# Kernel tuning notes

Hardware: AMD Instinct MI355X
Metric: run time of the kernel (lower is better)

Reference implementation:

```python
import jax, jax.numpy as jnp
import numpy as np

N, E, F, H, G, C, L = 50000, 800000, 128, 256, 128, 10, 3


def _gcn(x, src, dst, norm, W, b, n):
    # PyG GCNConv: h = x W; out_i = sum_{j->i} norm_ji h_j (+ self loops already in src/dst); + bias
    h = x @ W
    msg = h[src] * norm[:, None]              # [E+N, H]
    return jax.ops.segment_sum(msg, dst, num_segments=n) + b


def setup_inputs() -> dict:
    key = jax.random.key(0)
    ks = jax.random.split(key, 8)
    x = jax.random.normal(ks[0], (N, F), dtype=jnp.float32)
    edge_index = jax.random.randint(ks[1], (2, E), 0, N, dtype=jnp.int32)
    batch = jnp.sort(jax.random.randint(ks[2], (N,), 0, G, dtype=jnp.int32))
    graph_hidden = jax.random.normal(ks[3], (G, H), dtype=jnp.float32)
    W0 = jax.random.normal(ks[4], (F, H), dtype=jnp.float32) / np.sqrt(F)
    b0 = jnp.zeros((H,), jnp.float32)
    Ws = jax.random.normal(ks[5], (L, H, H), dtype=jnp.float32) / np.sqrt(H)
    bs = jnp.zeros((L, H), jnp.float32)
    Wlin = jax.random.normal(ks[6], (H, C), dtype=jnp.float32) / np.sqrt(H)
    blin = jnp.zeros((C,), jnp.float32)
    return {"x": x, "edge_index": edge_index, "batch": batch, "graph_hidden": graph_hidden,
            "W0": W0, "b0": b0, "Ws": Ws, "bs": bs, "Wlin": Wlin, "blin": blin}


def reference(x, edge_index, batch, graph_hidden, W0, b0, Ws, bs, Wlin, blin):
    n = x.shape[0]
    loops = jnp.arange(n, dtype=edge_index.dtype)
    src = jnp.concatenate([edge_index[0], loops])   # self loops appended
    dst = jnp.concatenate([edge_index[1], loops])
    deg = jax.ops.segment_sum(jnp.ones_like(src, dtype=x.dtype), dst, num_segments=n)
    inv_sqrt = jnp.where(deg > 0, jax.lax.rsqrt(deg), 0.0)
    norm = inv_sqrt[src] * inv_sqrt[dst]            # [E+N]

    h = _gcn(x, src, dst, norm, W0, b0, n)          # to_hidden (no activation, matches source)
    res = jax.lax.stop_gradient(graph_hidden[batch])  # no_grad residual, vectorized
    for i in range(Ws.shape[0]):
        h = h + res
        h = jax.nn.relu(_gcn(h, src, dst, norm, Ws[i], bs[i], n))
        # dropout is identity in eval mode

    counts = jax.ops.segment_sum(jnp.ones((n,), x.dtype), batch, num_segments=G)
    gm = jax.ops.segment_sum(h, batch, num_segments=G) / jnp.maximum(counts, 1.0)[:, None]
    gm = gm + graph_hidden
    y = gm @ Wlin + blin
    return (y, gm)
```

## Files before the change

kernel.cpp:

```cpp
#include <hip/hip_runtime.h>


typedef float f32x4 __attribute__((ext_vector_type(4)));
typedef float f32x2 __attribute__((ext_vector_type(2)));

__device__ inline float bf2f(unsigned short u) {
  union { unsigned int i; float f; } v;
  v.i = (unsigned int)u << 16;
  return v.f;
}
__device__ inline unsigned short f2bf(float f) {
  union { unsigned int i; float f; } v;
  v.f = f;
  unsigned int i = v.i;
  return (unsigned short)((i + 0x7fffu + ((i >> 16) & 1u)) >> 16);
}
__device__ inline unsigned pack4_fp8(float a, float b, float c, float d) {
  int r = 0;
  r = __builtin_amdgcn_cvt_pk_fp8_f32(a, b, r, false);
  r = __builtin_amdgcn_cvt_pk_fp8_f32(c, d, r, true);
  return (unsigned)r;
}
__device__ inline unsigned char f2fp8(float v) {
  return (unsigned char)((unsigned)__builtin_amdgcn_cvt_pk_fp8_f32(v, v, 0, false) & 0xffu);
}
__device__ inline void acc16_fp8(float* acc, uint4 r, unsigned msk) {
  unsigned w[4] = {r.x, r.y, r.z, r.w};
#pragma unroll
  for (int d = 0; d < 4; ++d) {
    int v = (int)(w[d] & msk);
    f32x2 lo = __builtin_amdgcn_cvt_pk_f32_fp8(v, false);
    f32x2 hi = __builtin_amdgcn_cvt_pk_f32_fp8(v, true);
    acc[4 * d + 0] += lo[0];
    acc[4 * d + 1] += lo[1];
    acc[4 * d + 2] += hi[0];
    acc[4 * d + 3] += hi[1];
  }
}
__device__ inline int lbound(const int* a, int n, int key) {
  int lo = 0, hi = n;
  while (lo < hi) {
    int mid = (lo + hi) >> 1;
    if (a[mid] < key) lo = mid + 1; else hi = mid;
  }
  return lo;
}


__global__ void count_pos_kernel(const int* __restrict__ dst, int* __restrict__ deg,
                                 unsigned short* __restrict__ pos, int E) {
  int e = blockIdx.x * blockDim.x + threadIdx.x;
  if (e < E) pos[e] = (unsigned short)atomicAdd(&deg[dst[e]], 1);
}

__global__ void scan_partial_kernel(const int* __restrict__ deg, float* __restrict__ inv_s,
                                    int* __restrict__ bsum, int N) {
  __shared__ int s[256];
  int i = blockIdx.x * 256 + threadIdx.x;
  int d = (i < N) ? deg[i] : 0;
  if (i < N) inv_s[i] = rsqrtf((float)(d + 1));
  s[threadIdx.x] = d;
  __syncthreads();
  for (int off = 128; off > 0; off >>= 1) {
    if (threadIdx.x < off) s[threadIdx.x] += s[threadIdx.x + off];
    __syncthreads();
  }
  if (threadIdx.x == 0) bsum[blockIdx.x] = s[0];
}

__global__ void scan_block_kernel(const int* __restrict__ bsum, int* __restrict__ boff,
                                  int* __restrict__ row_off, int NB, int N) {
  __shared__ int s[256];
  int v = (threadIdx.x < NB) ? bsum[threadIdx.x] : 0;
  s[threadIdx.x] = v;
  __syncthreads();
  for (int off = 1; off < 256; off <<= 1) {
    int t = (threadIdx.x >= off) ? s[threadIdx.x - off] : 0;
    __syncthreads();
    s[threadIdx.x] += t;
    __syncthreads();
  }
  boff[threadIdx.x] = s[threadIdx.x] - v;
  if (threadIdx.x == 255) row_off[N] = s[255];
}

__global__ void scan_final_kernel(const int* __restrict__ deg, const int* __restrict__ boff,
                                  int* __restrict__ row_off, int N) {
  __shared__ int s[256];
  int i = blockIdx.x * 256 + threadIdx.x;
  int v = (i < N) ? deg[i] : 0;
  s[threadIdx.x] = v;
  __syncthreads();
  for (int off = 1; off < 256; off <<= 1) {
    int t = (threadIdx.x >= off) ? s[threadIdx.x - off] : 0;
    __syncthreads();
    s[threadIdx.x] += t;
    __syncthreads();
  }
  if (i < N) row_off[i] = boff[blockIdx.x] + s[threadIdx.x] - v;
}

__global__ void fill_prep_kernel(const int* __restrict__ src, const int* __restrict__ dst,
                                 const unsigned short* __restrict__ pos,
                                 const int* __restrict__ row_off, int* __restrict__ col, int E,
                                 int FB, const float* __restrict__ x,
                                 const float* __restrict__ inv_s, unsigned* __restrict__ u,
                                 int total_dw, const float* __restrict__ W0,
                                 const float* __restrict__ Ws, unsigned char* __restrict__ Wt0,
                                 unsigned char* __restrict__ WtS) {
  const int FH = 128 * 256, HH = 256 * 256;
  int b = blockIdx.x;
  if (b < FB) {
    int t = b * 256 + threadIdx.x;
    int e = t * 4;
    if (e + 3 < E) {
      int4 s4 = *(const int4*)&src[e];
      int4 d4 = *(const int4*)&dst[e];
      ushort4 p4 = *(const ushort4*)&pos[e];
      col[row_off[d4.x] + p4.x] = s4.x;
      col[row_off[d4.y] + p4.y] = s4.y;
      col[row_off[d4.z] + p4.z] = s4.z;
      col[row_off[d4.w] + p4.w] = s4.w;
    } else {
      for (; e < E; ++e) col[row_off[dst[e]] + pos[e]] = src[e];
    }
  } else {
    int idx = (b - FB) * 256 + threadIdx.x;
    if (idx < total_dw) {
      int i = idx >> 5;
      float s = inv_s[i];
      float4 v = *(const float4*)&x[(size_t)idx * 4];
      u[idx] = pack4_fp8(s * v.x, s * v.y, s * v.z, s * v.w);
    } else {
      int w = idx - total_dw;
      if (w < FH) {
        int k = w >> 8, n = w & 255;
        Wt0[n * 128 + k] = f2fp8(W0[w]);
      } else {
        int t2 = w - FH;
        if (t2 < 3 * HH) {
          int l = t2 >> 16;
          int rem = t2 & 65535;
          int k = rem >> 8, n = rem & 255;
          WtS[l * HH + n * 256 + k] = f2fp8(Ws[t2]);
        }
      }
    }
  }
}

template <int CH>
__global__ __launch_bounds__(256) void aggregate_fp8_kernel(
    const unsigned char* __restrict__ u, const int* __restrict__ row_off,
    const int* __restrict__ col, const float* __restrict__ inv_s,
    unsigned char* __restrict__ out, int N) {
  constexpr int LPR = CH / 16;
  constexpr int EPW = 64 / LPR;
  int wave = threadIdx.x >> 6;
  int lane = threadIdx.x & 63;
  int i = blockIdx.x * 4 + wave;
  if (i >= N) return;
  int sub = lane / LPR;
  int c = lane % LPR;
  int e0 = row_off[i], e1 = row_off[i + 1];
  int last = e1 - 1;
  float acc[16] = {};
  for (int e = e0 + sub; e < e1; e += 4 * EPW) {
    unsigned off[4];
    unsigned msk[4];
#pragma unroll
    for (int q = 0; q < 4; ++q) {
      int ee = e + q * EPW;
      bool v = ee < e1;
      int j = col[v ? ee : last];
      off[q] = (unsigned)j * CH + c * 16;
      msk[q] = v ? 0xffffffffu : 0u;
    }
    uint4 r[4];
#pragma unroll
    for (int q = 0; q < 4; ++q) r[q] = *(const uint4*)(u + off[q]);
#pragma unroll
    for (int q = 0; q < 4; ++q) acc16_fp8(acc, r[q], msk[q]);
  }
#pragma unroll
  for (int o = 32; o >= LPR; o >>= 1)
#pragma unroll
    for (int k = 0; k < 16; ++k) acc[k] += __shfl_down(acc[k], o);
  if (lane < LPR) {
    uint4 self = *(const uint4*)(u + (size_t)i * CH + c * 16);
    acc16_fp8(acc, self, 0xffffffffu);
    float s = inv_s[i];
    uint4 o;
    o.x = pack4_fp8(s * acc[0], s * acc[1], s * acc[2], s * acc[3]);
    o.y = pack4_fp8(s * acc[4], s * acc[5], s * acc[6], s * acc[7]);
    o.z = pack4_fp8(s * acc[8], s * acc[9], s * acc[10], s * acc[11]);
    o.w = pack4_fp8(s * acc[12], s * acc[13], s * acc[14], s * acc[15]);
    *(uint4*)(out + (size_t)i * CH + c * 16) = o;
  }
}

__global__ __launch_bounds__(256) void aggregate_fp8_ns_kernel(
    const unsigned char* __restrict__ u, const int* __restrict__ row_off,
    const int* __restrict__ col, const float* __restrict__ inv_s,
    unsigned char* __restrict__ out, int N) {
  constexpr int CH = 256;
  int slice = blockIdx.x & 1;
  int nb = blockIdx.x >> 1;
  int lane = threadIdx.x & 63;
  int wave = threadIdx.x >> 6;
  int grp = lane >> 3;
  int c = lane & 7;
  int i = nb * 32 + wave * 8 + grp;
  if (i >= N) return;
  int e0 = row_off[i], e1 = row_off[i + 1];
  int last = e1 - 1;
  unsigned sofs = (unsigned)slice * 128 + c * 16;
  float acc[16] = {};
  for (int e = e0; e < e1; e += 4) {
    unsigned off[4];
    unsigned msk[4];
#pragma unroll
    for (int q = 0; q < 4; ++q) {
      int ee = e + q;
      bool v = ee < e1;
      int j = col[v ? ee : last];
      off[q] = (unsigned)j * CH + sofs;
      msk[q] = v ? 0xffffffffu : 0u;
    }
    uint4 r[4];
#pragma unroll
    for (int q = 0; q < 4; ++q) r[q] = *(const uint4*)(u + off[q]);
#pragma unroll
    for (int q = 0; q < 4; ++q) acc16_fp8(acc, r[q], msk[q]);
  }
  uint4 self = *(const uint4*)(u + (size_t)i * CH + sofs);
  acc16_fp8(acc, self, 0xffffffffu);
  float s = inv_s[i];
  uint4 o;
  o.x = pack4_fp8(s * acc[0], s * acc[1], s * acc[2], s * acc[3]);
  o.y = pack4_fp8(s * acc[4], s * acc[5], s * acc[6], s * acc[7]);
  o.z = pack4_fp8(s * acc[8], s * acc[9], s * acc[10], s * acc[11]);
  o.w = pack4_fp8(s * acc[12], s * acc[13], s * acc[14], s * acc[15]);
  *(uint4*)(out + (size_t)i * CH + sofs) = o;
}

template <int K, bool RELU, int OUTMODE>
__global__ __launch_bounds__(512) void gemm_kernel(
    const unsigned char* __restrict__ A,
    const unsigned char* __restrict__ Bt,
    const float* __restrict__ bias,
    const float* __restrict__ inv_s, const int* __restrict__ batch,
    const float* __restrict__ gh,
    void* __restrict__ outp,
    int M) {
  constexpr int BK = 64;
  constexpr int LDT = 80;
  __shared__ unsigned char As[128 * LDT];
  __shared__ unsigned char Bs[256 * LDT];
  int tid = threadIdx.x;
  int wave = tid >> 6, lane = tid & 63;
  int quad = lane >> 4, l15 = lane & 15;
  int wr = wave >> 2, wc = wave & 3;
  int row0 = blockIdx.x * 128;
  f32x4 acc[4][4];
#pragma unroll
  for (int m = 0; m < 4; ++m)
#pragma unroll
    for (int n = 0; n < 4; ++n) acc[m][n] = (f32x4){0.f, 0.f, 0.f, 0.f};

  for (int k0 = 0; k0 < K; k0 += BK) {
    {
      int r = tid >> 2, kq = tid & 3;
      int gr = row0 + r;
      uint4 v = make_uint4(0u, 0u, 0u, 0u);
      if (gr < M) v = *(const uint4*)&A[(size_t)gr * K + k0 + kq * 16];
      *(uint4*)&As[r * LDT + kq * 16] = v;
    }
#pragma unroll
    for (int p = 0; p < 2; ++p) {
      int n = (tid >> 2) + p * 128, kq = tid & 3;
      *(uint4*)&Bs[n * LDT + kq * 16] = *(const uint4*)&Bt[(size_t)n * K + k0 + kq * 16];
    }
    __syncthreads();
#pragma unroll
    for (int s = 0; s < 2; ++s) {
      long long af[4], bfr[4];
#pragma unroll
      for (int m = 0; m < 4; ++m)
        af[m] = *(const long long*)&As[(wr * 64 + m * 16 + l15) * LDT + s * 32 + quad * 8];
#pragma unroll
      for (int n = 0; n < 4; ++n)
        bfr[n] = *(const long long*)&Bs[(wc * 64 + n * 16 + l15) * LDT + s * 32 + quad * 8];
#pragma unroll
      for (int m = 0; m < 4; ++m)
#pragma unroll
        for (int n = 0; n < 4; ++n)
          acc[m][n] =
              __builtin_amdgcn_mfma_f32_16x16x32_fp8_fp8(af[m], bfr[n], acc[m][n], 0, 0, 0);
    }
    __syncthreads();
  }
  if (OUTMODE == 1) {
#pragma unroll
    for (int m = 0; m < 4; ++m) {
#pragma unroll
      for (int r = 0; r < 4; ++r) {
        int gr = row0 + wr * 64 + m * 16 + quad * 4 + r;
        if (gr >= M) continue;
        float sv = inv_s[gr];
        int bofs = batch[gr] * 256;
#pragma unroll
        for (int n = 0; n < 4; ++n) {
          int cc = wc * 64 + n * 16 + l15;
          float v = acc[m][n][r] + bias[cc];
          if (RELU) v = fmaxf(v, 0.f);
          v = sv * (v + gh[bofs + cc]);
          ((unsigned char*)outp)[(size_t)gr * 256 + cc] = f2fp8(v);
        }
      }
    }
  } else {
    float* gmsum = (float*)outp;
    float psum[4] = {0.f, 0.f, 0.f, 0.f};
    int cur_b = -1;
#pragma unroll
    for (int m = 0; m < 4; ++m) {
#pragma unroll
      for (int r = 0; r < 4; ++r) {
        int gr = row0 + wr * 64 + m * 16 + quad * 4 + r;
        if (gr >= M) continue;
        int b = batch[gr] * 256;
        if (b != cur_b) {
          if (cur_b >= 0) {
#pragma unroll
            for (int n = 0; n < 4; ++n)
              atomicAdd(&gmsum[cur_b + wc * 64 + n * 16 + l15], psum[n]);
          }
          cur_b = b;
#pragma unroll
          for (int n = 0; n < 4; ++n) psum[n] = 0.f;
        }
#pragma unroll
        for (int n = 0; n < 4; ++n) {
          int cc = wc * 64 + n * 16 + l15;
          float v = acc[m][n][r] + bias[cc];
          if (RELU) v = fmaxf(v, 0.f);
          psum[n] += v;
        }
      }
    }
    if (cur_b >= 0) {
#pragma unroll
      for (int n = 0; n < 4; ++n)
        atomicAdd(&gmsum[cur_b + wc * 64 + n * 16 + l15], psum[n]);
    }
  }
}


__global__ void final_kernel(const float* __restrict__ gmsum, const int* __restrict__ batch,
                             int N, const float* __restrict__ gh,
                             const float* __restrict__ Wlin, const float* __restrict__ blin,
                             float* __restrict__ y, float* __restrict__ gm_out, int G) {
  int g = blockIdx.x;
  int c = threadIdx.x;
  __shared__ float row[256];
  __shared__ int cnt_s;
  if (c == 0) cnt_s = lbound(batch, N, g + 1) - lbound(batch, N, g);
  __syncthreads();
  float v = gmsum[g * 256 + c] / fmaxf((float)cnt_s, 1.0f) + gh[g * 256 + c];
  gm_out[g * 256 + c] = v;
  row[c] = v;
  __syncthreads();
  if (c < 10) {
    float acc = blin[c];
    for (int k = 0; k < 256; ++k) acc += row[k] * Wlin[k * 10 + c];
    y[g * 10 + c] = acc;
  }
}


extern "C" void kernel_launch(void* const* d_in, const int* in_sizes, int n_in,
                              void* d_out, int out_size, void* d_ws, size_t ws_size,
                              hipStream_t stream) {
  const float* x = (const float*)d_in[0];
  const int* ei = (const int*)d_in[1];
  const int* batch = (const int*)d_in[2];
  const float* gh = (const float*)d_in[3];
  const float* W0 = (const float*)d_in[4];
  const float* b0 = (const float*)d_in[5];
  const float* Ws = (const float*)d_in[6];
  const float* bs = (const float*)d_in[7];
  const float* Wlin = (const float*)d_in[8];
  const float* blin = (const float*)d_in[9];
  float* out = (float*)d_out;

  const int N = in_sizes[2];
  const int E = in_sizes[1] / 2;
  const int G = in_sizes[3] / 256;
  const int H = 256, L = 3, C = 10, F = 128;

  char* ws = (char*)d_ws;
  size_t off = 0;
  auto alloc = [&](size_t bytes) {
    void* p = ws + off;
    off += (bytes + 255) & ~(size_t)255;
    return p;
  };
  int* deg = (int*)alloc((size_t)N * 4);
  float* gmsum = (float*)alloc((size_t)G * H * 4);
  int* row_off = (int*)alloc((size_t)(N + 1) * 4);
  int* bsum = (int*)alloc(256 * 4);
  int* boff = (int*)alloc(256 * 4);
  int* col = (int*)alloc((size_t)E * 4);
  unsigned short* pos = (unsigned short*)alloc((size_t)E * 2);
  float* inv_s = (float*)alloc((size_t)N * 4);
  unsigned char* u_x = (unsigned char*)alloc((size_t)N * F);
  unsigned char* uA = (unsigned char*)alloc((size_t)N * H);
  unsigned char* aggA = (unsigned char*)alloc((size_t)N * H);
  unsigned char* Wt0 = (unsigned char*)alloc((size_t)F * H);
  unsigned char* WtS = (unsigned char*)alloc((size_t)L * H * H);

  const int* srcv = ei;
  const int* dstv = ei + E;

  hipMemsetAsync(deg, 0, (size_t)N * 4, stream);
  hipMemsetAsync(gmsum, 0, (size_t)G * H * 4, stream);

  int EB = (E + 255) / 256;
  int NB = (N + 255) / 256;
  count_pos_kernel<<<EB, 256, 0, stream>>>(dstv, deg, pos, E);
  scan_partial_kernel<<<NB, 256, 0, stream>>>(deg, inv_s, bsum, N);
  scan_block_kernel<<<1, 256, 0, stream>>>(bsum, boff, row_off, NB, N);
  scan_final_kernel<<<NB, 256, 0, stream>>>(deg, boff, row_off, N);

  int FB = ((E + 3) / 4 + 255) / 256;
  int UXDW = N * (F / 4);
  int TW = F * H + 3 * H * H;
  int PREPB = (UXDW + TW + 255) / 256;
  fill_prep_kernel<<<FB + PREPB, 256, 0, stream>>>(srcv, dstv, pos, row_off, col, E, FB, x,
                                                   inv_s, (unsigned*)u_x, UXDW, W0, Ws, Wt0,
                                                   WtS);

  int AGG_GRID = (N + 3) / 4;
  int AGG_NS_GRID = ((N + 31) / 32) * 2;
  int GEMM_GRID = (N + 127) / 128;

  aggregate_fp8_kernel<128><<<AGG_GRID, 256, 0, stream>>>(u_x, row_off, col, inv_s, aggA, N);
  gemm_kernel<128, false, 1><<<GEMM_GRID, 512, 0, stream>>>(aggA, Wt0, b0, inv_s, batch, gh,
                                                            uA, N);
  for (int l = 0; l < 2; ++l) {
    aggregate_fp8_ns_kernel<<<AGG_NS_GRID, 256, 0, stream>>>(uA, row_off, col, inv_s, aggA, N);
    gemm_kernel<256, true, 1><<<GEMM_GRID, 512, 0, stream>>>(
        aggA, WtS + (size_t)l * H * H, bs + (size_t)l * H, inv_s, batch, gh, uA, N);
  }
  aggregate_fp8_ns_kernel<<<AGG_NS_GRID, 256, 0, stream>>>(uA, row_off, col, inv_s, aggA, N);
  gemm_kernel<256, true, 2><<<GEMM_GRID, 512, 0, stream>>>(
      aggA, WtS + (size_t)2 * H * H, bs + (size_t)2 * H, inv_s, batch, gh, gmsum, N);

  final_kernel<<<G, 256, 0, stream>>>(gmsum, batch, N, gh, Wlin, blin, out,
                                      out + (size_t)G * C, G);
}
```

Baseline: 367.0 us.

## Restructure first-layer aggregation to 8 lanes per node and fuse scan kernels

```diff
diff --git a/kernel.cpp b/kernel.cpp
--- a/kernel.cpp
+++ b/kernel.cpp
@@ -49,8 +49,19 @@
 
 __global__ void count_pos_kernel(const int* __restrict__ dst, int* __restrict__ deg,
                                  unsigned short* __restrict__ pos, int E) {
-  int e = blockIdx.x * blockDim.x + threadIdx.x;
-  if (e < E) pos[e] = (unsigned short)atomicAdd(&deg[dst[e]], 1);
+  int t = blockIdx.x * blockDim.x + threadIdx.x;
+  int e = t * 4;
+  if (e + 3 < E) {
+    int4 d4 = *(const int4*)&dst[e];
+    ushort4 p4;
+    p4.x = (unsigned short)atomicAdd(&deg[d4.x], 1);
+    p4.y = (unsigned short)atomicAdd(&deg[d4.y], 1);
+    p4.z = (unsigned short)atomicAdd(&deg[d4.z], 1);
+    p4.w = (unsigned short)atomicAdd(&deg[d4.w], 1);
+    *(ushort4*)&pos[e] = p4;
+  } else {
+    for (; e < E; ++e) pos[e] = (unsigned short)atomicAdd(&deg[dst[e]], 1);
+  }
 }
 
 __global__ void scan_partial_kernel(const int* __restrict__ deg, float* __restrict__ inv_s,
@@ -68,36 +79,32 @@
   if (threadIdx.x == 0) bsum[blockIdx.x] = s[0];
 }
 
-__global__ void scan_block_kernel(const int* __restrict__ bsum, int* __restrict__ boff,
+__global__ void scan_final_kernel(const int* __restrict__ deg, const int* __restrict__ bsum,
                                   int* __restrict__ row_off, int NB, int N) {
   __shared__ int s[256];
-  int v = (threadIdx.x < NB) ? bsum[threadIdx.x] : 0;
-  s[threadIdx.x] = v;
+  __shared__ int s2[256];
+  int tid = threadIdx.x;
+  int v2 = (tid < blockIdx.x && tid < NB) ? bsum[tid] : 0;
+  s2[tid] = v2;
+  __syncthreads();
+  for (int off = 128; off > 0; off >>= 1) {
+    if (tid < off) s2[tid] += s2[tid + off];
+    __syncthreads();
+  }
+  int boff = s2[0];
+  __syncthreads();
+  int i = blockIdx.x * 256 + tid;
+  int v = (i < N) ? deg[i] : 0;
+  s[tid] = v;
   __syncthreads();
   for (int off = 1; off < 256; off <<= 1) {
-    int t = (threadIdx.x >= off) ? s[threadIdx.x - off] : 0;
-    __syncthreads();
-    s[threadIdx.x] += t;
-    __syncthreads();
-  }
-  boff[threadIdx.x] = s[threadIdx.x] - v;
-  if (threadIdx.x == 255) row_off[N] = s[255];
-}
-
-__global__ void scan_final_kernel(const int* __restrict__ deg, const int* __restrict__ boff,
-                                  int* __restrict__ row_off, int N) {
-  __shared__ int s[256];
-  int i = blockIdx.x * 256 + threadIdx.x;
-  int v = (i < N) ? deg[i] : 0;
-  s[threadIdx.x] = v;
-  __syncthreads();
-  for (int off = 1; off < 256; off <<= 1) {
-    int t = (threadIdx.x >= off) ? s[threadIdx.x - off] : 0;
-    __syncthreads();
-    s[threadIdx.x] += t;
-    __syncthreads();
-  }
-  if (i < N) row_off[i] = boff[blockIdx.x] + s[threadIdx.x] - v;
+    int t = (tid >= off) ? s[tid - off] : 0;
+    __syncthreads();
+    s[tid] += t;
+    __syncthreads();
+  }
+  if (i < N) row_off[i] = boff + s[tid] - v;
+  if (blockIdx.x == NB - 1 && tid == 255) row_off[N] = boff + s[255];
 }
 
 __global__ void fill_prep_kernel(const int* __restrict__ src, const int* __restrict__ dst,
@@ -149,31 +156,30 @@
   }
 }
 
-template <int CH>
-__global__ __launch_bounds__(256) void aggregate_fp8_kernel(
+__global__ __launch_bounds__(256) void aggregate_fp8_ns128_kernel(
     const unsigned char* __restrict__ u, const int* __restrict__ row_off,
     const int* __restrict__ col, const float* __restrict__ inv_s,
     unsigned char* __restrict__ out, int N) {
-  constexpr int LPR = CH / 16;
-  constexpr int EPW = 64 / LPR;
+  constexpr int CH = 128;
+  int lane = threadIdx.x & 63;
   int wave = threadIdx.x >> 6;
-  int lane = threadIdx.x & 63;
-  int i = blockIdx.x * 4 + wave;
+  int grp = lane >> 3;
+  int c = lane & 7;
+  int i = blockIdx.x * 32 + wave * 8 + grp;
   if (i >= N) return;
-  int sub = lane / LPR;
-  int c = lane % LPR;
   int e0 = row_off[i], e1 = row_off[i + 1];
   int last = e1 - 1;
+  unsigned cofs = c * 16;
   float acc[16] = {};
-  for (int e = e0 + sub; e < e1; e += 4 * EPW) {
+  for (int e = e0; e < e1; e += 4) {
     unsigned off[4];
     unsigned msk[4];
 #pragma unroll
     for (int q = 0; q < 4; ++q) {
-      int ee = e + q * EPW;
+      int ee = e + q;
       bool v = ee < e1;
       int j = col[v ? ee : last];
-      off[q] = (unsigned)j * CH + c * 16;
+      off[q] = (unsigned)j * CH + cofs;
       msk[q] = v ? 0xffffffffu : 0u;
     }
     uint4 r[4];
@@ -182,21 +188,15 @@
 #pragma unroll
     for (int q = 0; q < 4; ++q) acc16_fp8(acc, r[q], msk[q]);
   }
-#pragma unroll
-  for (int o = 32; o >= LPR; o >>= 1)
-#pragma unroll
-    for (int k = 0; k < 16; ++k) acc[k] += __shfl_down(acc[k], o);
-  if (lane < LPR) {
-    uint4 self = *(const uint4*)(u + (size_t)i * CH + c * 16);
-    acc16_fp8(acc, self, 0xffffffffu);
-    float s = inv_s[i];
-    uint4 o;
-    o.x = pack4_fp8(s * acc[0], s * acc[1], s * acc[2], s * acc[3]);
-    o.y = pack4_fp8(s * acc[4], s * acc[5], s * acc[6], s * acc[7]);
-    o.z = pack4_fp8(s * acc[8], s * acc[9], s * acc[10], s * acc[11]);
-    o.w = pack4_fp8(s * acc[12], s * acc[13], s * acc[14], s * acc[15]);
-    *(uint4*)(out + (size_t)i * CH + c * 16) = o;
-  }
+  uint4 self = *(const uint4*)(u + (size_t)i * CH + cofs);
+  acc16_fp8(acc, self, 0xffffffffu);
+  float s = inv_s[i];
+  uint4 o;
+  o.x = pack4_fp8(s * acc[0], s * acc[1], s * acc[2], s * acc[3]);
+  o.y = pack4_fp8(s * acc[4], s * acc[5], s * acc[6], s * acc[7]);
+  o.z = pack4_fp8(s * acc[8], s * acc[9], s * acc[10], s * acc[11]);
+  o.w = pack4_fp8(s * acc[12], s * acc[13], s * acc[14], s * acc[15]);
+  *(uint4*)(out + (size_t)i * CH + cofs) = o;
 }
 
 __global__ __launch_bounds__(256) void aggregate_fp8_ns_kernel(
@@ -411,7 +411,6 @@
   float* gmsum = (float*)alloc((size_t)G * H * 4);
   int* row_off = (int*)alloc((size_t)(N + 1) * 4);
   int* bsum = (int*)alloc(256 * 4);
-  int* boff = (int*)alloc(256 * 4);
   int* col = (int*)alloc((size_t)E * 4);
   unsigned short* pos = (unsigned short*)alloc((size_t)E * 2);
   float* inv_s = (float*)alloc((size_t)N * 4);
@@ -427,12 +426,11 @@
   hipMemsetAsync(deg, 0, (size_t)N * 4, stream);
   hipMemsetAsync(gmsum, 0, (size_t)G * H * 4, stream);
 
-  int EB = (E + 255) / 256;
   int NB = (N + 255) / 256;
-  count_pos_kernel<<<EB, 256, 0, stream>>>(dstv, deg, pos, E);
+  int CPB = ((E + 3) / 4 + 255) / 256;
+  count_pos_kernel<<<CPB, 256, 0, stream>>>(dstv, deg, pos, E);
   scan_partial_kernel<<<NB, 256, 0, stream>>>(deg, inv_s, bsum, N);
-  scan_block_kernel<<<1, 256, 0, stream>>>(bsum, boff, row_off, NB, N);
-  scan_final_kernel<<<NB, 256, 0, stream>>>(deg, boff, row_off, N);
+  scan_final_kernel<<<NB, 256, 0, stream>>>(deg, bsum, row_off, NB, N);
 
   int FB = ((E + 3) / 4 + 255) / 256;
   int UXDW = N * (F / 4);
@@ -442,11 +440,11 @@
                                                    inv_s, (unsigned*)u_x, UXDW, W0, Ws, Wt0,
                                                    WtS);
 
-  int AGG_GRID = (N + 3) / 4;
+  int AGG0_GRID = (N + 31) / 32;
   int AGG_NS_GRID = ((N + 31) / 32) * 2;
   int GEMM_GRID = (N + 127) / 128;
 
-  aggregate_fp8_kernel<128><<<AGG_GRID, 256, 0, stream>>>(u_x, row_off, col, inv_s, aggA, N);
+  aggregate_fp8_ns128_kernel<<<AGG0_GRID, 256, 0, stream>>>(u_x, row_off, col, inv_s, aggA, N);
   gemm_kernel<128, false, 1><<<GEMM_GRID, 512, 0, stream>>>(aggA, Wt0, b0, inv_s, batch, gh,
                                                             uA, N);
   for (int l = 0; l < 2; ++l) {
```

New measurement: 355.9 us. 1.03x faster.
